# Optimization experiments

Hardware: AMD Instinct MI355X
Metric: run time of the kernel (lower is better)

Reference implementation:

```python
import jax, jax.numpy as jnp
import numpy as np
from jax.scipy.special import logsumexp

PAD_IDX, SOS_IDX, EOS_IDX = 0, 1, 2
NEG = -10000.0


def setup_inputs() -> dict:
    B, T, L = 64, 256, 8
    K, E, H = 128, 256, 512      # num_tags, EMBED_SIZE, HIDDEN_SIZE
    CV, WV = 128, 50000          # char / word vocab
    key = jax.random.key(0)
    ks = jax.random.split(key, 12)
    lengths = jax.random.randint(ks[0], (B,), T // 2, T + 1)
    mask = jnp.arange(T)[None, :] < lengths[:, None]          # [B,T] contiguous prefix
    wx = jnp.where(mask, jax.random.randint(ks[1], (B, T), 3, WV), 0).astype(jnp.int32)
    cx = jax.random.randint(ks[2], (B, T, L), 0, CV).astype(jnp.int32)
    y_body = jnp.where(mask, jax.random.randint(ks[3], (B, T), 3, K), PAD_IDX)
    y = jnp.concatenate([jnp.full((B, 1), SOS_IDX, jnp.int32), y_body.astype(jnp.int32)], 1)  # [B,T+1]
    s = 0.05
    char_emb = s * jax.random.normal(ks[4], (CV, E), jnp.float32)
    word_emb = s * jax.random.normal(ks[5], (WV, E), jnp.float32)
    Wi = s * jax.random.normal(ks[6], (E, 4 * H), jnp.float32)
    Wh = s * jax.random.normal(ks[7], (H, 4 * H), jnp.float32)
    b = jnp.zeros((4 * H,), jnp.float32)
    Wout = s * jax.random.normal(ks[8], (H, K), jnp.float32)
    bout = jnp.zeros((K,), jnp.float32)
    trans = jax.random.normal(ks[9], (K, K), jnp.float32)
    trans = trans.at[SOS_IDX, :].set(NEG)
    trans = trans.at[:, EOS_IDX].set(NEG)
    trans = trans.at[:, PAD_IDX].set(NEG)
    trans = trans.at[PAD_IDX, :].set(NEG)
    trans = trans.at[PAD_IDX, EOS_IDX].set(0.0)
    trans = trans.at[PAD_IDX, PAD_IDX].set(0.0)
    return dict(cx=cx, wx=wx, y=y, char_emb=char_emb, word_emb=word_emb,
                Wi=Wi, Wh=Wh, b=b, Wout=Wout, bout=bout, trans=trans)


def _forward(cx, wx, y, char_emb, word_emb, Wi, Wh, b, Wout, bout, trans):
    B, T = wx.shape
    K = trans.shape[0]
    H = Wh.shape[0]
    mask = (wx > 0)                                            # [B,T] bool
    maskf = mask.astype(jnp.float32)
    # embedding: word lookup + mean-pooled char lookup
    x = word_emb[wx] + char_emb[cx].mean(axis=2)               # [B,T,E]

    # masked LSTM (equivalent to pack_padded for prefix masks)
    def lstm_step(carry, inp):
        h, c = carry
        xt, mt = inp                                            # [B,E], [B,1]
        z = xt @ Wi + h @ Wh + b                                # [B,4H]
        i, f, g, o = jnp.split(z, 4, axis=-1)
        i, f, o = jax.nn.sigmoid(i), jax.nn.sigmoid(f), jax.nn.sigmoid(o)
        c_new = f * c + i * jnp.tanh(g)
        h_new = o * jnp.tanh(c_new)
        h = jnp.where(mt, h_new, h)
        c = jnp.where(mt, c_new, c)
        return (h, c), h

    h0 = jnp.zeros((B, H), x.dtype)
    xs = jnp.swapaxes(x, 0, 1)                                  # [T,B,E]
    ms = jnp.swapaxes(mask, 0, 1)[..., None]                    # [T,B,1]
    _, hs = jax.lax.scan(lstm_step, (h0, h0), (xs, ms))         # [T,B,H]
    hs = jnp.swapaxes(hs, 0, 1)                                 # [B,T,H]
    h = (hs @ Wout + bout) * maskf[..., None]                   # emissions [B,T,K]

    # CRF forward algorithm (log partition Z)
    score0 = jnp.full((B, K), NEG, h.dtype).at[:, SOS_IDX].set(0.0)

    def crf_step(score, inp):
        em, mt = inp                                            # [B,K], [B,1]
        s_t = logsumexp(score[:, None, :] + em[:, :, None] + trans[None, :, :], axis=-1)
        return jnp.where(mt, s_t, score), None

    emT = jnp.swapaxes(h, 0, 1)                                 # [T,B,K]
    scoreZ, _ = jax.lax.scan(crf_step, score0, (emT, ms))
    Z = logsumexp(scoreZ + trans[EOS_IDX], axis=-1)             # [B]

    # gold path score
    y_prev, y_next = y[:, :-1], y[:, 1:]                        # [B,T]
    emit = jnp.take_along_axis(h, y_next[..., None], axis=-1)[..., 0]  # [B,T]
    tr = trans[y_next, y_prev]                                  # [B,T]
    gold = jnp.sum((emit + tr) * maskf, axis=1)                 # [B]
    lengths = mask.sum(axis=1)
    last_tag = y[jnp.arange(B), lengths]                        # y has T+1 cols
    gold = gold + trans[EOS_IDX, last_tag]
    return Z - gold                                             # NLL per sequence [B]


def reference(cx, wx, y, char_emb, word_emb, Wi, Wh, b, Wout, bout, trans):
    return _forward(cx, wx, y, char_emb, word_emb, Wi, Wh, b, Wout, bout, trans)
```

## Files before the change

kernel.cpp:

```cpp
#include <hip/hip_runtime.h>


typedef float f32x4 __attribute__((ext_vector_type(4)));
typedef float f32x16 __attribute__((ext_vector_type(16)));
typedef __bf16 bf16x8 __attribute__((ext_vector_type(8)));
typedef unsigned int u32x4 __attribute__((ext_vector_type(4)));
typedef unsigned int u32x2 __attribute__((ext_vector_type(2)));

#define T_LEN 256
#define BB    64
#define EE    256
#define HH    512
#define KK    128
#define KCAT  768

static __device__ inline unsigned f2bf(float f) {
  union { float f; unsigned u; } v; v.f = f;
  unsigned r = v.u + 0x7FFF + ((v.u >> 16) & 1);
  return r >> 16;
}
static __device__ inline float sigm(float x) { return 1.f / (1.f + __expf(-x)); }
static __device__ inline float tanh_fast(float x) {
  return 1.f - 2.f / (1.f + __expf(2.f * x));
}
static __device__ inline bf16x8 ubf(u32x4 v) {
  union { u32x4 u; bf16x8 b; } c; c.u = v; return c.b;
}

__global__ __launch_bounds__(256) void build_wcat(
    const float* __restrict__ Wi, const float* __restrict__ Wh,
    unsigned short* __restrict__ WcatT) {
  __shared__ float tile[64][65];
  int ct = blockIdx.x & 31, kt = blockIdx.x >> 5;
  int tc = threadIdx.x & 63, tr = threadIdx.x >> 6;
  int c0 = ct * 64, k0 = kt * 64;
#pragma unroll
  for (int i = 0; i < 16; ++i) {
    int r = tr * 16 + i, k = k0 + r;
    float v = (k < EE) ? Wi[(size_t)k * 2048 + c0 + tc]
                       : Wh[(size_t)(k - EE) * 2048 + c0 + tc];
    tile[r][tc] = v;
  }
  __syncthreads();
#pragma unroll
  for (int i = 0; i < 16; ++i) {
    int cL = tr * 16 + i;
    WcatT[(size_t)(c0 + cL) * KCAT + k0 + tc] = (unsigned short)f2bf(tile[tc][cL]);
  }
}

__global__ __launch_bounds__(256) void build_wout(
    const float* __restrict__ Wout, unsigned short* __restrict__ WoutT) {
  __shared__ float tile[64][65];
  int ct = blockIdx.x & 1, kt = blockIdx.x >> 1;
  int tc = threadIdx.x & 63, tr = threadIdx.x >> 6;
  int c0 = ct * 64, k0 = kt * 64;
#pragma unroll
  for (int i = 0; i < 16; ++i) {
    int r = tr * 16 + i;
    tile[r][tc] = Wout[(size_t)(k0 + r) * KK + c0 + tc];
  }
  __syncthreads();
#pragma unroll
  for (int i = 0; i < 16; ++i) {
    int cL = tr * 16 + i;
    WoutT[(size_t)(c0 + cL) * HH + k0 + tc] = (unsigned short)f2bf(tile[tc][cL]);
  }
}

__global__ __launch_bounds__(256) void embed_kernel(
    const int* __restrict__ wx, const int* __restrict__ cx,
    const float* __restrict__ we, const float* __restrict__ ce,
    unsigned short* __restrict__ x) {
  int bid = blockIdx.x;
  int t = bid >> 6, b = bid & 63;
  int e = threadIdx.x;
  int w = wx[b * T_LEN + t];
  float v = we[(size_t)w * EE + e];
  const int* cp = cx + ((size_t)(b * T_LEN + t)) * 8;
  float s = 0.f;
#pragma unroll
  for (int l = 0; l < 8; ++l) s += ce[(size_t)cp[l] * EE + e];
  v += s * 0.125f;
  x[(size_t)bid * EE + e] = (unsigned short)f2bf(v);
}

__global__ void zero_flags(unsigned int* __restrict__ f) {
  int i = threadIdx.x;
  if (i < 320) {
    unsigned z = 0u;
    asm volatile("global_store_dword %0, %1, off sc1"
                 :: "v"(f + i), "v"(z) : "memory");
  }
}

#define SBAR __builtin_amdgcn_sched_barrier(0)
#define WAITV(N) do { asm volatile("s_waitcnt vmcnt(" #N ")" ::: "memory"); SBAR; } while (0)
#define LDN(dst, ptr, OFF) \
  asm volatile("global_load_dwordx4 %0, %1, off offset:" OFF \
               : "=v"(dst) : "v"(ptr) : "memory")

#define ISSUE_X(B, P) do { \
  LDN(B[0],P,"0");   LDN(B[1],P,"32");  LDN(B[2],P,"64");  LDN(B[3],P,"96"); \
  LDN(B[4],P,"128"); LDN(B[5],P,"160"); LDN(B[6],P,"192"); LDN(B[7],P,"224"); \
  LDN(B[8],P,"256"); LDN(B[9],P,"288"); LDN(B[10],P,"320"); LDN(B[11],P,"352"); \
  LDN(B[12],P,"384"); LDN(B[13],P,"416"); LDN(B[14],P,"448"); LDN(B[15],P,"480"); } while (0)
#define ISSUE_H1(B, P) do { \
  LDN(B[0],P,"512"); LDN(B[1],P,"544"); LDN(B[2],P,"576"); LDN(B[3],P,"608"); \
  LDN(B[4],P,"640"); LDN(B[5],P,"672"); LDN(B[6],P,"704"); LDN(B[7],P,"736"); \
  LDN(B[8],P,"768"); LDN(B[9],P,"800"); LDN(B[10],P,"832"); LDN(B[11],P,"864"); \
  LDN(B[12],P,"896"); LDN(B[13],P,"928"); LDN(B[14],P,"960"); LDN(B[15],P,"992"); } while (0)

#define GATES_STORE(T) do { \
    bool mk = ((int)wxv) > 0; \
    _Pragma("unroll") \
    for (int r = 0; r < 4; ++r) { \
      float zi = acc[r], zf = acc[4 + r], zg = acc[8 + r], zo = acc[12 + r]; \
      float cn = sigm(zf) * cst[r] + sigm(zi) * tanh_fast(zg); \
      float hn = sigm(zo) * tanh_fast(cn); \
      if (mk) { cst[r] = cn; hst[r] = hn; } \
    } \
    u32x2 ph; \
    ph[0] = f2bf(hst[0]) | (f2bf(hst[1]) << 16); \
    ph[1] = f2bf(hst[2]) | (f2bf(hst[3]) << 16); \
    asm volatile("global_store_dwordx2 %0, %1, off sc1" \
                 :: "v"(hstore + (size_t)(T) * 65536), "v"(ph) : "memory"); \
  } while (0)

__global__ __launch_bounds__(128, 1) void fused_kernel(
    const unsigned short* __restrict__ x,
    unsigned short* __restrict__ hs,
    const unsigned short* __restrict__ WcatT,
    const unsigned short* __restrict__ WoutT,
    const float* __restrict__ bias,
    const float* __restrict__ bout,
    const float* __restrict__ trans,
    const int* __restrict__ wx,
    const int* __restrict__ y,
    float* __restrict__ em,
    unsigned int* __restrict__ flags,
    unsigned int* __restrict__ emflag,
    float* __restrict__ out) {
  __shared__ float s_tl[KK][129];
  __shared__ float s_El[KK][129];
  __shared__ float s_p[KK];
  __shared__ float s_red[16];

  const int bid = blockIdx.x;
  const int tid = threadIdx.x;
  const int wave = tid >> 6, lane = tid & 63;

  if (bid < 64) {
    const int bhalf = wave;
    const int hi = lane >> 5;
    const int batch = bhalf * 32 + (lane & 31);
    const int u0 = bid * 8;
    const int rr = lane & 31;
    const int wcol = (rr >> 3) * HH + u0 + (rr & 7);

    bf16x8 wreg[48];
#pragma unroll
    for (int kf = 0; kf < 48; ++kf)
      wreg[kf] = *(const bf16x8*)(WcatT + (size_t)wcol * KCAT + kf * 16 + hi * 8);

    float bv[16];
#pragma unroll
    for (int q = 0; q < 4; ++q)
#pragma unroll
      for (int r = 0; r < 4; ++r)
        bv[q * 4 + r] = bias[q * HH + u0 + 4 * hi + r];

    const char* xlane  = (const char*)x  + ((size_t)batch * EE + hi * 8) * 2;
    const char* hread  = (const char*)hs + ((size_t)batch * HH + hi * 8) * 2;
    char*       hstore = (char*)hs + ((size_t)batch * HH + u0 + 4 * hi) * 2;
    const int*  wxp    = wx + batch * T_LEN;

    float cst[4] = {0.f, 0.f, 0.f, 0.f};
    float hst[4] = {0.f, 0.f, 0.f, 0.f};
    u32x4 bufX[16], bufH[16];
    unsigned wxv;
    f32x16 acc;

    ISSUE_X(bufX, xlane);
    asm volatile("global_load_dword %0, %1, off" : "=v"(wxv) : "v"(wxp) : "memory");
    WAITV(0);
#pragma unroll
    for (int i = 0; i < 16; ++i) acc[i] = bv[i];
#pragma unroll
    for (int kf = 0; kf < 16; ++kf)
      acc = __builtin_amdgcn_mfma_f32_32x32x16_bf16(wreg[kf], ubf(bufX[kf]), acc, 0, 0, 0);
    GATES_STORE(0);
    WAITV(0);
    __syncthreads();
    if (tid == 0)
      __hip_atomic_store(flags + bid, 1u, __ATOMIC_RELAXED, __HIP_MEMORY_SCOPE_AGENT);

    for (int t = 1; t < T_LEN; ++t) {
      const char* xt = xlane + (size_t)t * 32768;
      const char* hp = hread + (size_t)(t - 1) * 65536;

      ISSUE_X(bufX, xt);
      asm volatile("global_load_dword %0, %1, off" : "=v"(wxv) : "v"(wxp + t) : "memory");
      {
        unsigned v;
        do {
          asm volatile("global_load_dword %0, %1, off sc1\n\ts_waitcnt vmcnt(0)"
                       : "=v"(v) : "v"(flags + lane) : "memory");
        } while (!__all((int)(v >= (unsigned)t)));
        SBAR;
      }
      ISSUE_X(bufH, hp);
#pragma unroll
      for (int i = 0; i < 16; ++i) acc[i] = bv[i];
#pragma unroll
      for (int kf = 0; kf < 16; ++kf)
        acc = __builtin_amdgcn_mfma_f32_32x32x16_bf16(wreg[kf], ubf(bufX[kf]), acc, 0, 0, 0);
      SBAR;
      ISSUE_H1(bufX, hp);
      WAITV(16);
#pragma unroll
      for (int kf = 0; kf < 16; ++kf)
        acc = __builtin_amdgcn_mfma_f32_32x32x16_bf16(wreg[16 + kf], ubf(bufH[kf]), acc, 0, 0, 0);
      WAITV(0);
#pragma unroll
      for (int kf = 0; kf < 16; ++kf)
        acc = __builtin_amdgcn_mfma_f32_32x32x16_bf16(wreg[32 + kf], ubf(bufX[kf]), acc, 0, 0, 0);
      GATES_STORE(t);
      WAITV(0);
      __syncthreads();
      if (tid == 0)
        __hip_atomic_store(flags + bid, (unsigned)(t + 1),
                           __ATOMIC_RELAXED, __HIP_MEMORY_SCOPE_AGENT);
    }
  } else if (bid < 72) {
    const int et0 = bid - 64;
    const int arow = lane & 15, kg4 = (lane >> 4) * 8;
    for (int i = 0; i < 32; ++i) {
      const int t = et0 + 8 * i;
      {
        unsigned v; int it = 0;
        for (;;) {
          asm volatile("global_load_dword %0, %1, off sc1\n\ts_waitcnt vmcnt(0)"
                       : "=v"(v) : "v"(flags + lane) : "memory");
          if (__all((int)(v >= (unsigned)(t + 1)))) break;
          if (++it >= (1 << 17)) break;
          __builtin_amdgcn_s_sleep(2);
        }
        SBAR;
      }
      const unsigned short* A0 = hs + ((size_t)t * BB + wave * 32 + arow) * HH + kg4;
      f32x4 acc2[2][8];
#pragma unroll
      for (int mt = 0; mt < 2; ++mt)
#pragma unroll
        for (int nt = 0; nt < 8; ++nt) acc2[mt][nt] = (f32x4){0.f, 0.f, 0.f, 0.f};
#pragma unroll
      for (int ks = 0; ks < 16; ++ks) {
        bf16x8 a0 = *(const bf16x8*)(A0 + ks * 32);
        bf16x8 a1 = *(const bf16x8*)(A0 + 16 * HH + ks * 32);
#pragma unroll
        for (int nt = 0; nt < 8; ++nt) {
          bf16x8 bf = *(const bf16x8*)(WoutT + (size_t)(nt * 16 + arow) * HH + kg4 + ks * 32);
          acc2[0][nt] = __builtin_amdgcn_mfma_f32_16x16x32_bf16(a0, bf, acc2[0][nt], 0, 0, 0);
          acc2[1][nt] = __builtin_amdgcn_mfma_f32_16x16x32_bf16(a1, bf, acc2[1][nt], 0, 0, 0);
        }
      }
#pragma unroll
      for (int nt = 0; nt < 8; ++nt) {
        int n = nt * 16 + arow;
        float bo = bout[n];
#pragma unroll
        for (int mt = 0; mt < 2; ++mt)
#pragma unroll
          for (int r = 0; r < 4; ++r) {
            int row = t * BB + wave * 32 + mt * 16 + (lane >> 4) * 4 + r;
            float val = acc2[mt][nt][r] + bo;
            asm volatile("global_store_dword %0, %1, off sc1"
                         :: "v"(em + (size_t)row * KK + n), "v"(val) : "memory");
          }
      }
      WAITV(0);
      __syncthreads();
      if (tid == 0)
        __hip_atomic_store(emflag + t, 1u, __ATOMIC_RELAXED, __HIP_MEMORY_SCOPE_AGENT);
    }
  } else {
    const int b = bid - 72;
    const int k = tid;
    for (int i2 = tid; i2 < KK * KK; i2 += 128) {
      float v = trans[i2];
      s_tl[i2 >> 7][i2 & 127] = v;
      s_El[i2 >> 7][i2 & 127] = __expf(v);
    }
    __syncthreads();
    float sck = (k == 1) ? 0.f : -10000.f;
    float msc = 0.f;

    for (int t = 0; t < T_LEN; ++t) {
      if (wx[b * T_LEN + t] <= 0) continue;
      {
        unsigned v; int it = 0;
        for (;;) {
          asm volatile("global_load_dword %0, %1, off sc1\n\ts_waitcnt vmcnt(0)"
                       : "=v"(v) : "v"(emflag + t) : "memory");
          if (v) break;
          if (++it >= (1 << 17)) break;
          __builtin_amdgcn_s_sleep(2);
        }
        SBAR;
      }
      s_p[k] = __expf(sck - msc);
      __syncthreads();
      float S = 0.f;
#pragma unroll
      for (int j = 0; j < KK; ++j) S += s_El[k][j] * s_p[j];
      float ns = em[((size_t)t * BB + b) * KK + k] + msc + __logf(S);
      sck = ns;
      float m = ns;
#pragma unroll
      for (int off = 32; off; off >>= 1) m = fmaxf(m, __shfl_xor(m, off));
      if (lane == 0) s_red[8 + wave] = m;
      __syncthreads();
      msc = fmaxf(s_red[8], s_red[9]);
    }

    float term = 0.f, cnt = 0.f;
#pragma unroll
    for (int rep = 0; rep < 2; ++rep) {
      int tt = tid + rep * 128;
      int yp = y[b * 257 + tt], yn = y[b * 257 + tt + 1];
      if (wx[b * T_LEN + tt] > 0) {
        term += em[((size_t)tt * BB + b) * KK + yn] + s_tl[yn][yp];
        cnt += 1.f;
      }
    }
#pragma unroll
    for (int off = 32; off; off >>= 1) {
      term += __shfl_xor(term, off);
      cnt += __shfl_xor(cnt, off);
    }
    if (lane == 0) { s_red[wave] = term; s_red[2 + wave] = cnt; }
    __syncthreads();
    float gold = s_red[0] + s_red[1];
    int len = (int)(s_red[2] + s_red[3] + 0.5f);

    float v = sck + s_tl[2][k];
    float mz = v;
#pragma unroll
    for (int off = 32; off; off >>= 1) mz = fmaxf(mz, __shfl_xor(mz, off));
    if (lane == 0) s_red[4 + wave] = mz;
    __syncthreads();
    mz = fmaxf(s_red[4], s_red[5]);
    float e = __expf(v - mz);
#pragma unroll
    for (int off = 32; off; off >>= 1) e += __shfl_xor(e, off);
    if (lane == 0) s_red[6 + wave] = e;
    __syncthreads();
    if (tid == 0) {
      float Z = mz + __logf(s_red[6] + s_red[7]);
      int last_tag = y[b * 257 + len];
      out[b] = Z - (gold + s_tl[2][last_tag]);
    }
  }
}

extern "C" void kernel_launch(void* const* d_in, const int* in_sizes, int n_in,
                              void* d_out, int out_size, void* d_ws, size_t ws_size,
                              hipStream_t stream) {
  const int*   cx    = (const int*)d_in[0];
  const int*   wx    = (const int*)d_in[1];
  const int*   y     = (const int*)d_in[2];
  const float* ce    = (const float*)d_in[3];
  const float* we    = (const float*)d_in[4];
  const float* Wi    = (const float*)d_in[5];
  const float* Wh    = (const float*)d_in[6];
  const float* bias  = (const float*)d_in[7];
  const float* Wout  = (const float*)d_in[8];
  const float* bout  = (const float*)d_in[9];
  const float* trans = (const float*)d_in[10];
  float* out = (float*)d_out;

  char* ws = (char*)d_ws;
  unsigned short* WcatT = (unsigned short*)(ws + 0);
  unsigned short* WoutT = (unsigned short*)(ws + 3145728);
  unsigned short* x     = (unsigned short*)(ws + 3276800);
  unsigned short* hs    = (unsigned short*)(ws + 11665408);
  unsigned int*   flags = (unsigned int*)(ws + 28442624);
  unsigned int*   emflag= (unsigned int*)(ws + 28442880);
  float*          em    = (float*)(ws + 28444672);

  build_wcat<<<384, 256, 0, stream>>>(Wi, Wh, WcatT);
  build_wout<<<16, 256, 0, stream>>>(Wout, WoutT);
  embed_kernel<<<T_LEN * BB, 256, 0, stream>>>(wx, cx, we, ce, x);
  zero_flags<<<1, 320, 0, stream>>>(flags);
  fused_kernel<<<136, 128, 0, stream>>>(x, hs, WcatT, WoutT, bias, bout, trans,
                                        wx, y, em, flags, emflag, out);
}
```

Measured before the change: 1.448 ms.

## Fuse emission projection into CRF blocks and drop separate emission workers

Removes the eight MFMA-based emission blocks and the `em`/`emflag` handoff through global memory. Each CRF block now waits directly on the LSTM step flags, loads its own batch row of h into shared memory, and computes the 128 emissions with a scalar bf16 dot product per thread. Gold-path scoring is accumulated inside the recurrence, and the final reductions use shared-memory trees. This removes one producer/consumer hop and its global round-trip from the per-step chain. In exchange, each CRF step does a serial 512-long dot product per thread and rereads the Wout weights every step.

Result: slower. 3.485 ms (+140.7%).

```diff
diff --git a/kernel.cpp b/kernel.cpp
--- a/kernel.cpp
+++ b/kernel.cpp
@@ -18,6 +18,10 @@
   union { float f; unsigned u; } v; v.f = f;
   unsigned r = v.u + 0x7FFF + ((v.u >> 16) & 1);
   return r >> 16;
+}
+static __device__ inline float bf2f(unsigned short u) {
+  union { unsigned u; float f; } v; v.u = ((unsigned)u) << 16;
+  return v.f;
 }
 static __device__ inline float sigm(float x) { return 1.f / (1.f + __expf(-x)); }
 static __device__ inline float tanh_fast(float x) {
@@ -86,12 +90,9 @@
 }
 
 __global__ void zero_flags(unsigned int* __restrict__ f) {
-  int i = threadIdx.x;
-  if (i < 320) {
-    unsigned z = 0u;
-    asm volatile("global_store_dword %0, %1, off sc1"
-                 :: "v"(f + i), "v"(z) : "memory");
-  }
+  unsigned z = 0u;
+  asm volatile("global_store_dword %0, %1, off sc1"
+               :: "v"(f + threadIdx.x), "v"(z) : "memory");
 }
 
 #define SBAR __builtin_amdgcn_sched_barrier(0)
@@ -137,14 +138,13 @@
     const float* __restrict__ trans,
     const int* __restrict__ wx,
     const int* __restrict__ y,
-    float* __restrict__ em,
     unsigned int* __restrict__ flags,
-    unsigned int* __restrict__ emflag,
     float* __restrict__ out) {
-  __shared__ float s_tl[KK][129];
   __shared__ float s_El[KK][129];
+  __shared__ float s_h[HH];
   __shared__ float s_p[KK];
-  __shared__ float s_red[16];
+  __shared__ float s_red[4];
+  __shared__ float s_redg[KK];
 
   const int bid = blockIdx.x;
   const int tid = threadIdx.x;
@@ -232,11 +232,20 @@
         __hip_atomic_store(flags + bid, (unsigned)(t + 1),
                            __ATOMIC_RELAXED, __HIP_MEMORY_SCOPE_AGENT);
     }
-  } else if (bid < 72) {
-    const int et0 = bid - 64;
-    const int arow = lane & 15, kg4 = (lane >> 4) * 8;
-    for (int i = 0; i < 32; ++i) {
-      const int t = et0 + 8 * i;
+  } else {
+    const int b = bid - 64;
+    const int k = tid;
+    for (int i2 = tid; i2 < KK * KK; i2 += 128)
+      s_El[i2 >> 7][i2 & 127] = __expf(trans[i2]);
+    __syncthreads();
+
+    float sck = (k == 1) ? 0.f : -10000.f;
+    float msc = 0.f, gold = 0.f;
+    int len = 0;
+    const char* wp = (const char*)WoutT + (size_t)k * HH * 2;
+
+    for (int t = 0; t < T_LEN; ++t) {
+      if (wx[b * T_LEN + t] <= 0) continue;
       {
         unsigned v; int it = 0;
         for (;;) {
@@ -248,118 +257,72 @@
         }
         SBAR;
       }
-      const unsigned short* A0 = hs + ((size_t)t * BB + wave * 32 + arow) * HH + kg4;
-      f32x4 acc2[2][8];
-#pragma unroll
-      for (int mt = 0; mt < 2; ++mt)
-#pragma unroll
-        for (int nt = 0; nt < 8; ++nt) acc2[mt][nt] = (f32x4){0.f, 0.f, 0.f, 0.f};
-#pragma unroll
-      for (int ks = 0; ks < 16; ++ks) {
-        bf16x8 a0 = *(const bf16x8*)(A0 + ks * 32);
-        bf16x8 a1 = *(const bf16x8*)(A0 + 16 * HH + ks * 32);
-#pragma unroll
-        for (int nt = 0; nt < 8; ++nt) {
-          bf16x8 bf = *(const bf16x8*)(WoutT + (size_t)(nt * 16 + arow) * HH + kg4 + ks * 32);
-          acc2[0][nt] = __builtin_amdgcn_mfma_f32_16x16x32_bf16(a0, bf, acc2[0][nt], 0, 0, 0);
-          acc2[1][nt] = __builtin_amdgcn_mfma_f32_16x16x32_bf16(a1, bf, acc2[1][nt], 0, 0, 0);
+      {
+        u32x2 hv = *(const u32x2*)(hs + ((size_t)t * BB + b) * HH + tid * 4);
+        s_h[tid * 4]     = bf2f((unsigned short)(hv[0] & 0xffff));
+        s_h[tid * 4 + 1] = bf2f((unsigned short)(hv[0] >> 16));
+        s_h[tid * 4 + 2] = bf2f((unsigned short)(hv[1] & 0xffff));
+        s_h[tid * 4 + 3] = bf2f((unsigned short)(hv[1] >> 16));
+      }
+      __syncthreads();
+      float e = 0.f;
+#pragma unroll 16
+      for (int f = 0; f < 64; ++f) {
+        u32x4 wv = *(const u32x4*)(wp + f * 16);
+        const float* hb = s_h + f * 8;
+#pragma unroll
+        for (int d = 0; d < 4; ++d) {
+          e += hb[d * 2]     * bf2f((unsigned short)(wv[d] & 0xffff));
+          e += hb[d * 2 + 1] * bf2f((unsigned short)(wv[d] >> 16));
         }
       }
-#pragma unroll
-      for (int nt = 0; nt < 8; ++nt) {
-        int n = nt * 16 + arow;
-        float bo = bout[n];
-#pragma unroll
-        for (int mt = 0; mt < 2; ++mt)
-#pragma unroll
-          for (int r = 0; r < 4; ++r) {
-            int row = t * BB + wave * 32 + mt * 16 + (lane >> 4) * 4 + r;
-            float val = acc2[mt][nt][r] + bo;
-            asm volatile("global_store_dword %0, %1, off sc1"
-                         :: "v"(em + (size_t)row * KK + n), "v"(val) : "memory");
-          }
-      }
-      WAITV(0);
-      __syncthreads();
-      if (tid == 0)
-        __hip_atomic_store(emflag + t, 1u, __ATOMIC_RELAXED, __HIP_MEMORY_SCOPE_AGENT);
-    }
-  } else {
-    const int b = bid - 72;
-    const int k = tid;
-    for (int i2 = tid; i2 < KK * KK; i2 += 128) {
-      float v = trans[i2];
-      s_tl[i2 >> 7][i2 & 127] = v;
-      s_El[i2 >> 7][i2 & 127] = __expf(v);
-    }
-    __syncthreads();
-    float sck = (k == 1) ? 0.f : -10000.f;
-    float msc = 0.f;
-
-    for (int t = 0; t < T_LEN; ++t) {
-      if (wx[b * T_LEN + t] <= 0) continue;
-      {
-        unsigned v; int it = 0;
-        for (;;) {
-          asm volatile("global_load_dword %0, %1, off sc1\n\ts_waitcnt vmcnt(0)"
-                       : "=v"(v) : "v"(emflag + t) : "memory");
-          if (v) break;
-          if (++it >= (1 << 17)) break;
-          __builtin_amdgcn_s_sleep(2);
-        }
-        SBAR;
-      }
+      float em_k = e + bout[k];
       s_p[k] = __expf(sck - msc);
       __syncthreads();
       float S = 0.f;
 #pragma unroll
       for (int j = 0; j < KK; ++j) S += s_El[k][j] * s_p[j];
-      float ns = em[((size_t)t * BB + b) * KK + k] + msc + __logf(S);
+      float ns = em_k + msc + __logf(S);
+      int yn = y[b * 257 + t + 1];
+      if (k == yn) gold += em_k + trans[yn * KK + y[b * 257 + t]];
+      len++;
       sck = ns;
       float m = ns;
 #pragma unroll
       for (int off = 32; off; off >>= 1) m = fmaxf(m, __shfl_xor(m, off));
-      if (lane == 0) s_red[8 + wave] = m;
-      __syncthreads();
-      msc = fmaxf(s_red[8], s_red[9]);
-    }
-
-    float term = 0.f, cnt = 0.f;
-#pragma unroll
-    for (int rep = 0; rep < 2; ++rep) {
-      int tt = tid + rep * 128;
-      int yp = y[b * 257 + tt], yn = y[b * 257 + tt + 1];
-      if (wx[b * T_LEN + tt] > 0) {
-        term += em[((size_t)tt * BB + b) * KK + yn] + s_tl[yn][yp];
-        cnt += 1.f;
-      }
-    }
-#pragma unroll
-    for (int off = 32; off; off >>= 1) {
-      term += __shfl_xor(term, off);
-      cnt += __shfl_xor(cnt, off);
-    }
-    if (lane == 0) { s_red[wave] = term; s_red[2 + wave] = cnt; }
-    __syncthreads();
-    float gold = s_red[0] + s_red[1];
-    int len = (int)(s_red[2] + s_red[3] + 0.5f);
-
-    float v = sck + s_tl[2][k];
-    float mz = v;
-#pragma unroll
-    for (int off = 32; off; off >>= 1) mz = fmaxf(mz, __shfl_xor(mz, off));
-    if (lane == 0) s_red[4 + wave] = mz;
-    __syncthreads();
-    mz = fmaxf(s_red[4], s_red[5]);
-    float e = __expf(v - mz);
-#pragma unroll
-    for (int off = 32; off; off >>= 1) e += __shfl_xor(e, off);
-    if (lane == 0) s_red[6 + wave] = e;
-    __syncthreads();
+      if (lane == 0) s_red[wave] = m;
+      __syncthreads();
+      msc = fmaxf(s_red[0], s_red[1]);
+    }
+
+    s_redg[tid] = gold;
+    __syncthreads();
+    for (int s2 = 64; s2 > 0; s2 >>= 1) {
+      if (tid < s2) s_redg[tid] += s_redg[tid + s2];
+      __syncthreads();
+    }
+    gold = s_redg[0];
+    __syncthreads();
+
+    float v = sck + trans[2 * KK + k];
+    s_redg[tid] = v;
+    __syncthreads();
+    for (int s2 = 64; s2 > 0; s2 >>= 1) {
+      if (tid < s2) s_redg[tid] = fmaxf(s_redg[tid], s_redg[tid + s2]);
+      __syncthreads();
+    }
+    float mz = s_redg[0];
+    __syncthreads();
+    s_redg[tid] = __expf(v - mz);
+    __syncthreads();
+    for (int s2 = 64; s2 > 0; s2 >>= 1) {
+      if (tid < s2) s_redg[tid] += s_redg[tid + s2];
+      __syncthreads();
+    }
     if (tid == 0) {
-      float Z = mz + __logf(s_red[6] + s_red[7]);
+      float Z = mz + __logf(s_redg[0]);
       int last_tag = y[b * 257 + len];
-      out[b] = Z - (gold + s_tl[2][last_tag]);
+      out[b] = Z - (gold + trans[2 * KK + last_tag]);
     }
   }
 }
@@ -386,13 +349,11 @@
   unsigned short* x     = (unsigned short*)(ws + 3276800);
   unsigned short* hs    = (unsigned short*)(ws + 11665408);
   unsigned int*   flags = (unsigned int*)(ws + 28442624);
-  unsigned int*   emflag= (unsigned int*)(ws + 28442880);
-  float*          em    = (float*)(ws + 28444672);
 
   build_wcat<<<384, 256, 0, stream>>>(Wi, Wh, WcatT);
   build_wout<<<16, 256, 0, stream>>>(Wout, WoutT);
   embed_kernel<<<T_LEN * BB, 256, 0, stream>>>(wx, cx, we, ce, x);
-  zero_flags<<<1, 320, 0, stream>>>(flags);
-  fused_kernel<<<136, 128, 0, stream>>>(x, hs, WcatT, WoutT, bias, bout, trans,
-                                        wx, y, em, flags, emflag, out);
-}
+  zero_flags<<<1, 64, 0, stream>>>(flags);
+  fused_kernel<<<128, 128, 0, stream>>>(x, hs, WcatT, WoutT, bias, bout, trans,
+                                        wx, y, flags, out);
+}
```
